# Optimization experiments

Measured on AMD Instinct MI355X. Metric: run time of the kernel, lower is better.

## Reference

```python
import jax, jax.numpy as jnp
import numpy as np

B, D, K = 32768, 1024, 64
N3, N4, N5 = 512, 512, 512


def setup_inputs() -> dict:
    key = jax.random.key(0)
    ks = jax.random.split(key, 10)
    # x in [-1, 1]^D as the docstring states
    x = jax.random.uniform(ks[0], (B, D), dtype=jnp.float32, minval=-1.0, maxval=1.0)
    S = jnp.sort(jax.random.randint(ks[1], (K,), 0, D, dtype=jnp.int32))
    a = jax.random.normal(ks[2], (K,), dtype=jnp.float32)
    b = jax.random.normal(ks[3], (K, K), dtype=jnp.float32)
    idx3 = jax.random.randint(ks[4], (N3, 3), 0, K, dtype=jnp.int32)
    c3 = jax.random.normal(ks[5], (N3,), dtype=jnp.float32)
    idx4 = jax.random.randint(ks[6], (N4, 4), 0, K, dtype=jnp.int32)
    c4 = jax.random.normal(ks[7], (N4,), dtype=jnp.float32)
    idx5 = jax.random.randint(ks[8], (N5, 5), 0, K, dtype=jnp.int32)
    c5 = jax.random.normal(ks[9], (N5,), dtype=jnp.float32)
    return {"x": x, "S": S, "a": a, "b": b, "idx3": idx3, "c3": c3,
            "idx4": idx4, "c4": c4, "idx5": idx5, "c5": c5}


def _monomial_term(xS, idx, c):
    # xS: (B,k); idx: (n,deg); c: (n,) -> (B,)
    # gather -> (B, n, deg), product over monomial factors, weighted sum
    prod = jnp.prod(xS[:, idx], axis=2)  # (B, n)
    return prod @ c


def reference(x, S, a, b, idx3, c3, idx4, c4, idx5, c5):
    xS = x[:, S]                      # (B, k)
    lin = xS @ a                      # (B,)
    # sum_{i<j} b[i,j] xS_i xS_j == einsum with strictly-upper-triangular b
    bu = jnp.triu(b, k=1)             # (k, k)
    quad = jnp.einsum('bi,ij,bj->b', xS, bu, xS)
    out = lin + quad
    out = out + _monomial_term(xS, idx3, c3)
    out = out + _monomial_term(xS, idx4, c4)
    out = out + _monomial_term(xS, idx5, c5)
    return out
```

## Files before the change

kernel.cpp:

```cpp
#include <hip/hip_runtime.h>
#include <hip/hip_fp16.h>
#include <stdint.h>

#define NT 256
#define RPB 32
#define XSTR 80

#define WS_P3   0
#define WS_P4   4096
#define WS_P5   12288
#define WS_BUTH 20480

static __device__ __forceinline__ __half2 H2(unsigned u) {
    return __builtin_bit_cast(__half2, u);
}
static __device__ __forceinline__ unsigned short f2hbits(float f) {
    __half h = __float2half(f);
    return __builtin_bit_cast(unsigned short, h);
}

__global__ void prepack(const float* __restrict__ b,
                        const int* __restrict__ i3, const float* __restrict__ c3,
                        const int* __restrict__ i4, const float* __restrict__ c4,
                        const int* __restrict__ i5, const float* __restrict__ c5,
                        unsigned char* __restrict__ ws)
{
    const int g = blockIdx.x * NT + threadIdx.x;
    if (g < 4096) {
        const int i = g >> 6, j = g & 63;
        float v = (i < j) ? b[g] : 0.0f;
        ((unsigned short*)(ws + WS_BUTH))[(i >> 3) * 512 + j * 8 + (i & 7)] = f2hbits(v);
    }
    if (g < 512) {
        const int slot = (g & 63) * 8 + (g >> 6);
        unsigned o0, o1, o2, o3, o4;
        o0 = (unsigned)i3[3*g+0] * XSTR; o1 = (unsigned)i3[3*g+1] * XSTR; o2 = (unsigned)i3[3*g+2] * XSTR;
        ((uint2*)(ws + WS_P3))[slot] = make_uint2(o0 | (o1 << 16), o2 | ((unsigned)f2hbits(c3[g]) << 16));
        o0 = (unsigned)i4[4*g+0] * XSTR; o1 = (unsigned)i4[4*g+1] * XSTR;
        o2 = (unsigned)i4[4*g+2] * XSTR; o3 = (unsigned)i4[4*g+3] * XSTR;
        ((uint4*)(ws + WS_P4))[slot] = make_uint4(o0 | (o1 << 16), o2 | (o3 << 16), (unsigned)f2hbits(c4[g]), 0u);
        o0 = (unsigned)i5[5*g+0] * XSTR; o1 = (unsigned)i5[5*g+1] * XSTR;
        o2 = (unsigned)i5[5*g+2] * XSTR; o3 = (unsigned)i5[5*g+3] * XSTR;
        o4 = (unsigned)i5[5*g+4] * XSTR;
        ((uint4*)(ws + WS_P5))[slot] = make_uint4(o0 | (o1 << 16), o2 | (o3 << 16), o4 | ((unsigned)f2hbits(c5[g]) << 16), 0u);
    }
}

static __device__ __forceinline__ void qfma(__half2 bb, uint4 xk, __half2 d[4]) {
    d[0] = __hfma2(bb, H2(xk.x), d[0]);
    d[1] = __hfma2(bb, H2(xk.y), d[1]);
    d[2] = __hfma2(bb, H2(xk.z), d[2]);
    d[3] = __hfma2(bb, H2(xk.w), d[3]);
}
static __device__ __forceinline__ void pmul(const uint4& a, __half2 p[4]) {
    p[0] = __hmul2(p[0], H2(a.x));
    p[1] = __hmul2(p[1], H2(a.y));
    p[2] = __hmul2(p[2], H2(a.z));
    p[3] = __hmul2(p[3], H2(a.w));
}
static __device__ __forceinline__ void pacc(__half2 c2, const __half2 p[4], __half2 acc[4]) {
    acc[0] = __hfma2(c2, p[0], acc[0]);
    acc[1] = __hfma2(c2, p[1], acc[1]);
    acc[2] = __hfma2(c2, p[2], acc[2]);
    acc[3] = __hfma2(c2, p[3], acc[3]);
}

__global__ __launch_bounds__(NT, 4)
void poly_main(const float* __restrict__ x, const int* __restrict__ S,
               const float* __restrict__ a,
               const unsigned char* __restrict__ ws, float* __restrict__ out)
{
    __shared__ __align__(16) __half xS[64 * 40];
    __shared__ __align__(16) unsigned char buT2[8192];
    __shared__ float red[4][4][8];

    const int tid  = threadIdx.x;
    const int row0 = blockIdx.x * RPB;

    const int rg = tid & 3;
    const int ts = tid >> 2;

    const int k = tid & 63, q = tid >> 6;
    const int sk = S[k];
    const float* xc = x + (size_t)row0 * 1024 + sk;
    float v[8];
    #pragma unroll
    for (int m = 0; m < 8; ++m) v[m] = xc[(size_t)(q * 8 + m) * 1024];

    uint2 e3[8];
    uint4 e4[8], e5[8];
    {
        const uint4* s3 = (const uint4*)(ws + WS_P3 + ts * 64);
        #pragma unroll
        for (int i = 0; i < 4; ++i) ((uint4*)e3)[i] = s3[i];
        const uint4* s4 = (const uint4*)(ws + WS_P4 + ts * 128);
        #pragma unroll
        for (int i = 0; i < 8; ++i) e4[i] = s4[i];
        const uint4* s5 = (const uint4*)(ws + WS_P5 + ts * 128);
        #pragma unroll
        for (int i = 0; i < 8; ++i) e5[i] = s5[i];
    }
    const float av = a[ts];

    {
        const uint4* src = (const uint4*)(ws + WS_BUTH);
        uint4* dst = (uint4*)buT2;
        dst[tid]       = src[tid];
        dst[tid + 256] = src[tid + 256];
    }

    {
        uint4 pk;
        pk.x = __builtin_bit_cast(unsigned, __floats2half2_rn(v[0], v[1]));
        pk.y = __builtin_bit_cast(unsigned, __floats2half2_rn(v[2], v[3]));
        pk.z = __builtin_bit_cast(unsigned, __floats2half2_rn(v[4], v[5]));
        pk.w = __builtin_bit_cast(unsigned, __floats2half2_rn(v[6], v[7]));
        *(uint4*)((char*)xS + k * XSTR + q * 16) = pk;
    }
    __syncthreads();

    const char* xb = (const char*)xS + rg * 16;

    __half2 d[4] = {H2(0u), H2(0u), H2(0u), H2(0u)};
    {
        const int nii = (ts + 7) >> 3;
        #pragma unroll
        for (int g = 0; g < 8; ++g) {
            if (g < nii) {
                uint4 w4 = *(const uint4*)(buT2 + g * 1024 + ts * 16);
                const char* xkb = xb + g * 8 * XSTR;
                unsigned pw[4] = {w4.x, w4.y, w4.z, w4.w};
                #pragma unroll
                for (int p = 0; p < 4; ++p) {
                    __half2 blo = __half2half2(__ushort_as_half((unsigned short)(pw[p] & 0xFFFFu)));
                    __half2 bhi = __half2half2(__ushort_as_half((unsigned short)(pw[p] >> 16)));
                    uint4 x0 = *(const uint4*)(xkb + (2 * p + 0) * XSTR);
                    uint4 x1 = *(const uint4*)(xkb + (2 * p + 1) * XSTR);
                    qfma(blo, x0, d);
                    qfma(bhi, x1, d);
                }
            }
        }
    }
    __half2 acc[4];
    {
        __half2 a2 = __half2half2(__float2half(av));
        uint4 xj = *(const uint4*)(xb + ts * XSTR);
        acc[0] = __hmul2(__hadd2(a2, d[0]), H2(xj.x));
        acc[1] = __hmul2(__hadd2(a2, d[1]), H2(xj.y));
        acc[2] = __hmul2(__hadd2(a2, d[2]), H2(xj.z));
        acc[3] = __hmul2(__hadd2(a2, d[3]), H2(xj.w));
    }

    #pragma unroll
    for (int m = 0; m < 8; ++m) {
        uint2 p = e3[m];
        uint4 v0 = *(const uint4*)(xb + (p.x & 0xFFFFu));
        uint4 v1 = *(const uint4*)(xb + (p.x >> 16));
        uint4 v2 = *(const uint4*)(xb + (p.y & 0xFFFFu));
        __half2 pr[4] = {H2(v0.x), H2(v0.y), H2(v0.z), H2(v0.w)};
        pmul(v1, pr);
        pmul(v2, pr);
        pacc(__half2half2(__ushort_as_half((unsigned short)(p.y >> 16))), pr, acc);
    }
    #pragma unroll
    for (int m = 0; m < 8; ++m) {
        uint4 p = e4[m];
        uint4 v0 = *(const uint4*)(xb + (p.x & 0xFFFFu));
        uint4 v1 = *(const uint4*)(xb + (p.x >> 16));
        uint4 v2 = *(const uint4*)(xb + (p.y & 0xFFFFu));
        uint4 v3 = *(const uint4*)(xb + (p.y >> 16));
        __half2 pr[4] = {H2(v0.x), H2(v0.y), H2(v0.z), H2(v0.w)};
        pmul(v1, pr);
        pmul(v2, pr);
        pmul(v3, pr);
        pacc(__half2half2(__ushort_as_half((unsigned short)(p.z & 0xFFFFu))), pr, acc);
    }
    #pragma unroll
    for (int m = 0; m < 8; ++m) {
        uint4 p = e5[m];
        uint4 v0 = *(const uint4*)(xb + (p.x & 0xFFFFu));
        uint4 v1 = *(const uint4*)(xb + (p.x >> 16));
        uint4 v2 = *(const uint4*)(xb + (p.y & 0xFFFFu));
        uint4 v3 = *(const uint4*)(xb + (p.y >> 16));
        uint4 v4 = *(const uint4*)(xb + (p.z & 0xFFFFu));
        __half2 pr[4] = {H2(v0.x), H2(v0.y), H2(v0.z), H2(v0.w)};
        pmul(v1, pr);
        pmul(v2, pr);
        pmul(v3, pr);
        pmul(v4, pr);
        pacc(__half2half2(__ushort_as_half((unsigned short)(p.z >> 16))), pr, acc);
    }

    float f[8];
    #pragma unroll
    for (int e = 0; e < 4; ++e) {
        f[2 * e]     = __low2float(acc[e]);
        f[2 * e + 1] = __high2float(acc[e]);
    }
    #pragma unroll
    for (int mask = 4; mask <= 32; mask <<= 1) {
        #pragma unroll
        for (int r = 0; r < 8; ++r) f[r] += __shfl_xor(f[r], mask, 64);
    }
    const int w = tid >> 6, lane = tid & 63;
    if (lane < 4) {
        #pragma unroll
        for (int r = 0; r < 8; ++r) red[w][lane][r] = f[r];
    }
    __syncthreads();
    if (tid < 32) {
        int g = tid >> 3, e = tid & 7;
        out[row0 + tid] = red[0][g][e] + red[1][g][e] + red[2][g][e] + red[3][g][e];
    }
}

extern "C" void kernel_launch(void* const* d_in, const int* in_sizes, int n_in,
                              void* d_out, int out_size, void* d_ws, size_t ws_size,
                              hipStream_t stream) {
    const float* x  = (const float*)d_in[0];
    const int*   S  = (const int*)d_in[1];
    const float* a  = (const float*)d_in[2];
    const float* b  = (const float*)d_in[3];
    const int*   i3 = (const int*)d_in[4];
    const float* c3 = (const float*)d_in[5];
    const int*   i4 = (const int*)d_in[6];
    const float* c4 = (const float*)d_in[7];
    const int*   i5 = (const int*)d_in[8];
    const float* c5 = (const float*)d_in[9];
    unsigned char* ws = (unsigned char*)d_ws;
    float* out = (float*)d_out;

    prepack<<<16, NT, 0, stream>>>(b, i3, c3, i4, c4, i5, c5, ws);
    poly_main<<<32768 / RPB, NT, 0, stream>>>(x, S, a, ws, out);
}
```

Baseline: 206.9 us.

## Process two 32-row slabs per block with prefetch of the next slab

Each block now handles 64 rows as two 32-row stages. The global loads for the second slab are issued before computing the first slab and written into a second shared buffer afterward, so gather latency overlaps with compute. This also amortizes the per-block setup (monomial descriptor loads into registers, b-matrix copy into shared memory) over twice as many rows, at the cost of half as many blocks, more shared memory, and extra registers for the prefetched values.

```diff
diff --git a/kernel.cpp b/kernel.cpp
--- a/kernel.cpp
+++ b/kernel.cpp
@@ -3,7 +3,8 @@
 #include <stdint.h>
 
 #define NT 256
-#define RPB 32
+#define RPB 64
+#define SROWS 32
 #define XSTR 80
 
 #define WS_P3   0
@@ -70,9 +71,9 @@
                const float* __restrict__ a,
                const unsigned char* __restrict__ ws, float* __restrict__ out)
 {
-    __shared__ __align__(16) __half xS[64 * 40];
+    __shared__ __align__(16) __half xS[2][64 * 40];
     __shared__ __align__(16) unsigned char buT2[8192];
-    __shared__ float red[4][4][8];
+    __shared__ float red[2][4][4][8];
 
     const int tid  = threadIdx.x;
     const int row0 = blockIdx.x * RPB;
@@ -115,103 +116,124 @@
         pk.y = __builtin_bit_cast(unsigned, __floats2half2_rn(v[2], v[3]));
         pk.z = __builtin_bit_cast(unsigned, __floats2half2_rn(v[4], v[5]));
         pk.w = __builtin_bit_cast(unsigned, __floats2half2_rn(v[6], v[7]));
-        *(uint4*)((char*)xS + k * XSTR + q * 16) = pk;
+        *(uint4*)((char*)xS[0] + k * XSTR + q * 16) = pk;
     }
     __syncthreads();
 
-    const char* xb = (const char*)xS + rg * 16;
-
-    __half2 d[4] = {H2(0u), H2(0u), H2(0u), H2(0u)};
-    {
-        const int nii = (ts + 7) >> 3;
-        #pragma unroll
-        for (int g = 0; g < 8; ++g) {
-            if (g < nii) {
-                uint4 w4 = *(const uint4*)(buT2 + g * 1024 + ts * 16);
-                const char* xkb = xb + g * 8 * XSTR;
-                unsigned pw[4] = {w4.x, w4.y, w4.z, w4.w};
-                #pragma unroll
-                for (int p = 0; p < 4; ++p) {
-                    __half2 blo = __half2half2(__ushort_as_half((unsigned short)(pw[p] & 0xFFFFu)));
-                    __half2 bhi = __half2half2(__ushort_as_half((unsigned short)(pw[p] >> 16)));
-                    uint4 x0 = *(const uint4*)(xkb + (2 * p + 0) * XSTR);
-                    uint4 x1 = *(const uint4*)(xkb + (2 * p + 1) * XSTR);
-                    qfma(blo, x0, d);
-                    qfma(bhi, x1, d);
+    #pragma unroll
+    for (int s = 0; s < 2; ++s) {
+        float vn[8];
+        if (s == 0) {
+            const float* xc1 = xc + (size_t)SROWS * 1024;
+            #pragma unroll
+            for (int m = 0; m < 8; ++m) vn[m] = xc1[(size_t)(q * 8 + m) * 1024];
+        }
+
+        const char* xb = (const char*)xS[s] + rg * 16;
+
+        __half2 d[4] = {H2(0u), H2(0u), H2(0u), H2(0u)};
+        {
+            const int nii = (ts + 7) >> 3;
+            #pragma unroll
+            for (int g = 0; g < 8; ++g) {
+                if (g < nii) {
+                    uint4 w4 = *(const uint4*)(buT2 + g * 1024 + ts * 16);
+                    const char* xkb = xb + g * 8 * XSTR;
+                    unsigned pw[4] = {w4.x, w4.y, w4.z, w4.w};
+                    #pragma unroll
+                    for (int p = 0; p < 4; ++p) {
+                        __half2 blo = __half2half2(__ushort_as_half((unsigned short)(pw[p] & 0xFFFFu)));
+                        __half2 bhi = __half2half2(__ushort_as_half((unsigned short)(pw[p] >> 16)));
+                        uint4 x0 = *(const uint4*)(xkb + (2 * p + 0) * XSTR);
+                        uint4 x1 = *(const uint4*)(xkb + (2 * p + 1) * XSTR);
+                        qfma(blo, x0, d);
+                        qfma(bhi, x1, d);
+                    }
                 }
             }
         }
-    }
-    __half2 acc[4];
-    {
-        __half2 a2 = __half2half2(__float2half(av));
-        uint4 xj = *(const uint4*)(xb + ts * XSTR);
-        acc[0] = __hmul2(__hadd2(a2, d[0]), H2(xj.x));
-        acc[1] = __hmul2(__hadd2(a2, d[1]), H2(xj.y));
-        acc[2] = __hmul2(__hadd2(a2, d[2]), H2(xj.z));
-        acc[3] = __hmul2(__hadd2(a2, d[3]), H2(xj.w));
-    }
-
-    #pragma unroll
-    for (int m = 0; m < 8; ++m) {
-        uint2 p = e3[m];
-        uint4 v0 = *(const uint4*)(xb + (p.x & 0xFFFFu));
-        uint4 v1 = *(const uint4*)(xb + (p.x >> 16));
-        uint4 v2 = *(const uint4*)(xb + (p.y & 0xFFFFu));
-        __half2 pr[4] = {H2(v0.x), H2(v0.y), H2(v0.z), H2(v0.w)};
-        pmul(v1, pr);
-        pmul(v2, pr);
-        pacc(__half2half2(__ushort_as_half((unsigned short)(p.y >> 16))), pr, acc);
-    }
-    #pragma unroll
-    for (int m = 0; m < 8; ++m) {
-        uint4 p = e4[m];
-        uint4 v0 = *(const uint4*)(xb + (p.x & 0xFFFFu));
-        uint4 v1 = *(const uint4*)(xb + (p.x >> 16));
-        uint4 v2 = *(const uint4*)(xb + (p.y & 0xFFFFu));
-        uint4 v3 = *(const uint4*)(xb + (p.y >> 16));
-        __half2 pr[4] = {H2(v0.x), H2(v0.y), H2(v0.z), H2(v0.w)};
-        pmul(v1, pr);
-        pmul(v2, pr);
-        pmul(v3, pr);
-        pacc(__half2half2(__ushort_as_half((unsigned short)(p.z & 0xFFFFu))), pr, acc);
-    }
-    #pragma unroll
-    for (int m = 0; m < 8; ++m) {
-        uint4 p = e5[m];
-        uint4 v0 = *(const uint4*)(xb + (p.x & 0xFFFFu));
-        uint4 v1 = *(const uint4*)(xb + (p.x >> 16));
-        uint4 v2 = *(const uint4*)(xb + (p.y & 0xFFFFu));
-        uint4 v3 = *(const uint4*)(xb + (p.y >> 16));
-        uint4 v4 = *(const uint4*)(xb + (p.z & 0xFFFFu));
-        __half2 pr[4] = {H2(v0.x), H2(v0.y), H2(v0.z), H2(v0.w)};
-        pmul(v1, pr);
-        pmul(v2, pr);
-        pmul(v3, pr);
-        pmul(v4, pr);
-        pacc(__half2half2(__ushort_as_half((unsigned short)(p.z >> 16))), pr, acc);
-    }
-
-    float f[8];
-    #pragma unroll
-    for (int e = 0; e < 4; ++e) {
-        f[2 * e]     = __low2float(acc[e]);
-        f[2 * e + 1] = __high2float(acc[e]);
-    }
-    #pragma unroll
-    for (int mask = 4; mask <= 32; mask <<= 1) {
-        #pragma unroll
-        for (int r = 0; r < 8; ++r) f[r] += __shfl_xor(f[r], mask, 64);
-    }
-    const int w = tid >> 6, lane = tid & 63;
-    if (lane < 4) {
-        #pragma unroll
-        for (int r = 0; r < 8; ++r) red[w][lane][r] = f[r];
-    }
-    __syncthreads();
-    if (tid < 32) {
-        int g = tid >> 3, e = tid & 7;
-        out[row0 + tid] = red[0][g][e] + red[1][g][e] + red[2][g][e] + red[3][g][e];
+        __half2 acc[4];
+        {
+            __half2 a2 = __half2half2(__float2half(av));
+            uint4 xj = *(const uint4*)(xb + ts * XSTR);
+            acc[0] = __hmul2(__hadd2(a2, d[0]), H2(xj.x));
+            acc[1] = __hmul2(__hadd2(a2, d[1]), H2(xj.y));
+            acc[2] = __hmul2(__hadd2(a2, d[2]), H2(xj.z));
+            acc[3] = __hmul2(__hadd2(a2, d[3]), H2(xj.w));
+        }
+
+        #pragma unroll
+        for (int m = 0; m < 8; ++m) {
+            uint2 p = e3[m];
+            uint4 v0 = *(const uint4*)(xb + (p.x & 0xFFFFu));
+            uint4 v1 = *(const uint4*)(xb + (p.x >> 16));
+            uint4 v2 = *(const uint4*)(xb + (p.y & 0xFFFFu));
+            __half2 pr[4] = {H2(v0.x), H2(v0.y), H2(v0.z), H2(v0.w)};
+            pmul(v1, pr);
+            pmul(v2, pr);
+            pacc(__half2half2(__ushort_as_half((unsigned short)(p.y >> 16))), pr, acc);
+        }
+        #pragma unroll
+        for (int m = 0; m < 8; ++m) {
+            uint4 p = e4[m];
+            uint4 v0 = *(const uint4*)(xb + (p.x & 0xFFFFu));
+            uint4 v1 = *(const uint4*)(xb + (p.x >> 16));
+            uint4 v2 = *(const uint4*)(xb + (p.y & 0xFFFFu));
+            uint4 v3 = *(const uint4*)(xb + (p.y >> 16));
+            __half2 pr[4] = {H2(v0.x), H2(v0.y), H2(v0.z), H2(v0.w)};
+            pmul(v1, pr);
+            pmul(v2, pr);
+            pmul(v3, pr);
+            pacc(__half2half2(__ushort_as_half((unsigned short)(p.z & 0xFFFFu))), pr, acc);
+        }
+        #pragma unroll
+        for (int m = 0; m < 8; ++m) {
+            uint4 p = e5[m];
+            uint4 v0 = *(const uint4*)(xb + (p.x & 0xFFFFu));
+            uint4 v1 = *(const uint4*)(xb + (p.x >> 16));
+            uint4 v2 = *(const uint4*)(xb + (p.y & 0xFFFFu));
+            uint4 v3 = *(const uint4*)(xb + (p.y >> 16));
+            uint4 v4 = *(const uint4*)(xb + (p.z & 0xFFFFu));
+            __half2 pr[4] = {H2(v0.x), H2(v0.y), H2(v0.z), H2(v0.w)};
+            pmul(v1, pr);
+            pmul(v2, pr);
+            pmul(v3, pr);
+            pmul(v4, pr);
+            pacc(__half2half2(__ushort_as_half((unsigned short)(p.z >> 16))), pr, acc);
+        }
+
+        float f[8];
+        #pragma unroll
+        for (int e = 0; e < 4; ++e) {
+            f[2 * e]     = __low2float(acc[e]);
+            f[2 * e + 1] = __high2float(acc[e]);
+        }
+        #pragma unroll
+        for (int mask = 4; mask <= 32; mask <<= 1) {
+            #pragma unroll
+            for (int r = 0; r < 8; ++r) f[r] += __shfl_xor(f[r], mask, 64);
+        }
+
+        if (s == 0) {
+            uint4 pk;
+            pk.x = __builtin_bit_cast(unsigned, __floats2half2_rn(vn[0], vn[1]));
+            pk.y = __builtin_bit_cast(unsigned, __floats2half2_rn(vn[2], vn[3]));
+            pk.z = __builtin_bit_cast(unsigned, __floats2half2_rn(vn[4], vn[5]));
+            pk.w = __builtin_bit_cast(unsigned, __floats2half2_rn(vn[6], vn[7]));
+            *(uint4*)((char*)xS[1] + k * XSTR + q * 16) = pk;
+        }
+
+        const int w = tid >> 6, lane = tid & 63;
+        if (lane < 4) {
+            #pragma unroll
+            for (int r = 0; r < 8; ++r) red[s][w][lane][r] = f[r];
+        }
+        __syncthreads();
+        if (tid < 32) {
+            int g = tid >> 3, e = tid & 7;
+            out[row0 + s * SROWS + tid] =
+                red[s][0][g][e] + red[s][1][g][e] + red[s][2][g][e] + red[s][3][g][e];
+        }
     }
 }
 
```

Measured after the change: 216.5 us. 4.6% more time.
